# Kernel tuning notes

Hardware: AMD Instinct MI355X
Metric: run time of the kernel (lower is better)

The kernel has to match this reference:

```python
import jax, jax.numpy as jnp
import numpy as np

K = 3          # kernel size
PAD = 1        # padding
KK = K * K
RECURRENT = 3  # opt.Recurrent_times - 1


def dcnv2(x, offset, mask, weight, bias):
    """Modulated deformable conv (DCNv2), stride 1, pad 1, dilation 1.

    x:      [B, C, H, W]
    offset: [B, 2*KK, H, W]  -- (dy, dx) interleaved per kernel tap
    mask:   [B, KK, H, W]    -- modulation scalars
    weight: [O, C, K, K], bias: [O]
    """
    B, C, H, W = x.shape
    off = offset.reshape(B, KK, 2, H, W)
    dy, dx = off[:, :, 0], off[:, :, 1]                       # [B,KK,H,W]

    ky, kx = jnp.meshgrid(jnp.arange(K), jnp.arange(K), indexing='ij')
    ky = (ky.reshape(KK) - PAD).astype(x.dtype)               # {-1,0,1}
    kx = (kx.reshape(KK) - PAD).astype(x.dtype)
    iy = jnp.arange(H, dtype=x.dtype)
    ix = jnp.arange(W, dtype=x.dtype)

    # fractional sampling coords, [B,KK,H,W]
    py = iy[None, None, :, None] + ky[None, :, None, None] + dy
    px = ix[None, None, None, :] + kx[None, :, None, None] + dx

    y0 = jnp.floor(py)
    x0 = jnp.floor(px)
    wy = (py - y0)[:, None]                                   # [B,1,KK,H,W]
    wx = (px - x0)[:, None]

    x_flat = x.reshape(B, C, H * W)

    def gather(yi, xi):
        valid = ((yi >= 0) & (yi <= H - 1) & (xi >= 0) & (xi <= W - 1))
        yc = jnp.clip(yi, 0, H - 1).astype(jnp.int32)
        xc = jnp.clip(xi, 0, W - 1).astype(jnp.int32)
        idx = (yc * W + xc).reshape(B, -1)                    # [B, KK*H*W]
        g = jax.vmap(lambda im, id_: im[:, id_])(x_flat, idx)  # [B,C,KK*H*W]
        return g.reshape(B, C, KK, H, W) * valid.astype(x.dtype)[:, None]

    v00 = gather(y0, x0)
    v01 = gather(y0, x0 + 1)
    v10 = gather(y0 + 1, x0)
    v11 = gather(y0 + 1, x0 + 1)

    val = (v00 * (1 - wy) * (1 - wx) + v01 * (1 - wy) * wx
           + v10 * wy * (1 - wx) + v11 * wy * wx)
    val = val * mask[:, None]                                  # modulation

    out = jnp.einsum('ock,bckhw->bohw', weight.reshape(weight.shape[0], C, KK), val)
    return out + bias[None, :, None, None]


def setup_inputs() -> dict:
    key = jax.random.key(0)
    k1, k2, k3 = jax.random.split(key, 3)
    B, H, W = 4, 512, 512
    sharp = jax.random.normal(k1, (B, 3, H, W), dtype=jnp.float32)
    motion = jax.random.normal(k2, (B, 3 * KK, H, W), dtype=jnp.float32)
    # one 3x3x3->3 conv per recurrence, stacked: [RECURRENT, O, C, K, K]
    dcn_weights = jax.random.normal(k3, (RECURRENT, 3, 3, K, K), dtype=jnp.float32) * 0.1
    dcn_biases = jnp.zeros((RECURRENT, 3), dtype=jnp.float32)
    return {"sharp": sharp, "motion": motion,
            "dcn_weights": dcn_weights, "dcn_biases": dcn_biases}


def reference(sharp, motion, dcn_weights, dcn_biases):
    # torch.split(motion, [2*KK, KK], dim=1)
    offset = motion[:, :2 * KK]
    mask = motion[:, 2 * KK:]
    feats = [sharp]
    cur = sharp
    for i in range(RECURRENT):
        cur = dcnv2(cur, offset, mask, dcn_weights[i], dcn_biases[i])
        feats.append(cur)
    return sum(feats) / (RECURRENT + 1)
```

## Files before the change

kernel.cpp:

```cpp
#include <hip/hip_runtime.h>
#include <hip/hip_fp16.h>


#define HH 512
#define WW 512
#define BATCH 4
#define HWSZ (HH * WW)
#define PAIRS_PER_IMG (HWSZ / 2)

union U4 { uint4 u; __half2 h[4]; };
union U2 { uint2 u; __half2 h[2]; };

typedef const __attribute__((address_space(1))) void* gas_t;
typedef __attribute__((address_space(3))) void* las_t;

__global__ __launch_bounds__(256) void to_half_kernel(
    const float* __restrict__ sharp, uint4* __restrict__ dst)
{
    const int i = blockIdx.x * 256 + threadIdx.x;
    const int b = i >> 17;
    const int p = (i & (PAIRS_PER_IMG - 1)) * 2;
    const float* s = sharp + (size_t)b * 3 * HWSZ + p;
    const float2 c0 = *(const float2*)(s);
    const float2 c1 = *(const float2*)(s + HWSZ);
    const float2 c2 = *(const float2*)(s + 2 * HWSZ);
    U4 o;
    o.h[0] = __float22half2_rn(make_float2(c0.x, c1.x));
    o.h[1] = __float22half2_rn(make_float2(c2.x, 0.f));
    o.h[2] = __float22half2_rn(make_float2(c0.y, c1.y));
    o.h[3] = __float22half2_rn(make_float2(c2.y, 0.f));
    dst[i] = o.u;
}

__device__ __forceinline__ void bilinear3(const char* __restrict__ sb,
                                          float py, float px, float m,
                                          float& o0, float& o1, float& o2)
{
    const float y0f = floorf(py), x0f = floorf(px);
    const float wy = py - y0f, wx = px - x0f;
    const bool vy0 = (y0f >= 0.f) && (y0f <= 511.f);
    const bool vy1 = (y0f >= -1.f) && (y0f <= 510.f);
    const bool vx0 = (x0f >= 0.f) && (x0f <= 511.f);
    const bool vx1 = (x0f >= -1.f) && (x0f <= 510.f);
    const int iy0 = (int)fminf(fmaxf(y0f, 0.f), 511.f);
    const int iy1 = (int)fminf(fmaxf(y0f + 1.f, 0.f), 511.f);
    const int ix0 = (int)fminf(fmaxf(x0f, 0.f), 511.f);
    const int ix1 = (int)fminf(fmaxf(x0f + 1.f, 0.f), 511.f);
    const int lc  = (int)fminf(fmaxf(x0f, 0.f), 510.f);
    const int s0 = ix0 - lc;
    const int s1 = ix1 - lc;

    const float w00 = (vy0 && vx0) ? (1.f - wy) * (1.f - wx) * m : 0.f;
    const float w01 = (vy0 && vx1) ? (1.f - wy) * wx * m : 0.f;
    const float w10 = (vy1 && vx0) ? wy * (1.f - wx) * m : 0.f;
    const float w11 = (vy1 && vx1) ? wy * wx * m : 0.f;

    const float wlo0 = s0 ? 0.f : (s1 ? w00 : w00 + w01);
    const float whi0 = s1 ? (s0 ? w00 + w01 : w01) : 0.f;
    const float wlo1 = s0 ? 0.f : (s1 ? w10 : w10 + w11);
    const float whi1 = s1 ? (s0 ? w10 + w11 : w11) : 0.f;

    U4 ra, rb;
    ra.u = *(const uint4*)(sb + (size_t)(iy0 * WW + lc) * 8);
    rb.u = *(const uint4*)(sb + (size_t)(iy1 * WW + lc) * 8);
    const float2 aL = __half22float2(ra.h[0]);
    const float2 aLz = __half22float2(ra.h[1]);
    const float2 aH = __half22float2(ra.h[2]);
    const float2 aHz = __half22float2(ra.h[3]);
    const float2 bL = __half22float2(rb.h[0]);
    const float2 bLz = __half22float2(rb.h[1]);
    const float2 bH = __half22float2(rb.h[2]);
    const float2 bHz = __half22float2(rb.h[3]);

    o0 = wlo0 * aL.x + whi0 * aH.x + wlo1 * bL.x + whi1 * bH.x;
    o1 = wlo0 * aL.y + whi0 * aH.y + wlo1 * bL.y + whi1 * bH.y;
    o2 = wlo0 * aLz.x + whi0 * aHz.x + wlo1 * bLz.x + whi1 * bHz.x;
}

template <bool FIRST, bool WRITE_DST>
__global__ __launch_bounds__(256) void dcn_kernel(
    const uint2* __restrict__ src,
    const float* __restrict__ motion,
    const float* __restrict__ wgt,
    const float* __restrict__ bias,
    uint2* __restrict__ dst,
    float* __restrict__ out)
{
    __shared__ float mlds[27][256];
    __shared__ float sw[84];

    const int t = threadIdx.x;
    const int blk = blockIdx.x;
    const int b = blk >> 10;
    const int pbase = (blk & 1023) * 256;
    const int p = pbase + t;
    const int y = p >> 9;
    const int x = p & 511;

    if (t < 84) sw[t] = (t < 81) ? wgt[t] : bias[t - 81];

    {
        const int w = t >> 6, lane = t & 63;
        const float* mbase = motion + (size_t)b * 27 * HWSZ + pbase;
#pragma unroll
        for (int r = 0; r < 7; ++r) {
            const int plane = r * 4 + w;
            if (plane < 27) {
                const float* gsrc = mbase + (size_t)plane * HWSZ + lane * 4;
                __builtin_amdgcn_global_load_lds((gas_t)gsrc,
                                                 (las_t)&mlds[plane][0],
                                                 16, 0, 0);
            }
        }
    }
    __syncthreads();

    const char* sb = (const char*)src + (size_t)b * HWSZ * 8;

    float acc0 = sw[81], acc1 = sw[82], acc2 = sw[83];

#pragma unroll
    for (int k = 0; k < 9; ++k) {
        const float dy = mlds[2 * k][t];
        const float dx = mlds[2 * k + 1][t];
        const float m  = mlds[18 + k][t];
        const float py = (float)(y + k / 3 - 1) + dy;
        const float px = (float)(x + k % 3 - 1) + dx;

        float v0, v1, v2;
        bilinear3(sb, py, px, m, v0, v1, v2);
        acc0 += sw[0 * 9 + k] * v0 + sw[1 * 9 + k] * v1 + sw[2 * 9 + k] * v2;
        acc1 += sw[3 * 9 + k] * v0 + sw[4 * 9 + k] * v1 + sw[5 * 9 + k] * v2;
        acc2 += sw[6 * 9 + k] * v0 + sw[7 * 9 + k] * v1 + sw[8 * 9 + k] * v2;
    }

    if (WRITE_DST) {
        U2 o;
        o.h[0] = __float22half2_rn(make_float2(acc0, acc1));
        o.h[1] = __float22half2_rn(make_float2(acc2, 0.f));
        dst[(size_t)b * HWSZ + p] = o.u;
    }

    const size_t ob = (size_t)b * 3 * HWSZ + p;
    if (FIRST) {
        U2 c;
        c.u = *(const uint2*)(sb + (size_t)p * 8);
        const float2 s01 = __half22float2(c.h[0]);
        const float2 s2 = __half22float2(c.h[1]);
        out[ob] = (s01.x + acc0) * 0.25f;
        out[ob + HWSZ] = (s01.y + acc1) * 0.25f;
        out[ob + 2 * HWSZ] = (s2.x + acc2) * 0.25f;
    } else {
        out[ob] += acc0 * 0.25f;
        out[ob + HWSZ] += acc1 * 0.25f;
        out[ob + 2 * HWSZ] += acc2 * 0.25f;
    }
}

extern "C" void kernel_launch(void* const* d_in, const int* in_sizes, int n_in,
                              void* d_out, int out_size, void* d_ws, size_t ws_size,
                              hipStream_t stream) {
    const float* sharp  = (const float*)d_in[0];
    const float* motion = (const float*)d_in[1];
    const float* wts    = (const float*)d_in[2];
    const float* bias   = (const float*)d_in[3];
    float* out = (float*)d_out;

    uint2* bufA = (uint2*)d_ws;
    uint2* bufB = bufA + (size_t)BATCH * HWSZ;

    const dim3 block(256);
    const dim3 gridT(BATCH * PAIRS_PER_IMG / 256);
    const dim3 gridD(BATCH * HWSZ / 256);

    to_half_kernel<<<gridT, block, 0, stream>>>(sharp, (uint4*)bufA);
    dcn_kernel<true, true><<<gridD, block, 0, stream>>>(
        bufA, motion, wts, bias, bufB, out);
    dcn_kernel<false, true><<<gridD, block, 0, stream>>>(
        bufB, motion, wts + 81, bias + 3, bufA, out);
    dcn_kernel<false, false><<<gridD, block, 0, stream>>>(
        bufA, motion, wts + 162, bias + 6, nullptr, out);
}
```

Baseline: 119.5 us.

## Stage source halo tile in LDS and defer output accumulation to last pass

Each block now loads a 10x266 halo tile of the half-precision source image into shared memory and takes its bilinear samples from it, falling back to global loads when an offset points outside the tile. The output read-modify-write in every pass is replaced by writing three intermediate fp16 buffers, and the last pass sums them all into the output once. This cuts scattered global gather traffic and the repeated fp32 output reads and writes. In exchange it adds tile-loading work, more shared memory per block, a divergent fallback path, and extra fp16 buffer reads in the final pass.

```diff
diff --git a/kernel.cpp b/kernel.cpp
--- a/kernel.cpp
+++ b/kernel.cpp
@@ -6,7 +6,12 @@
 #define WW 512
 #define BATCH 4
 #define HWSZ (HH * WW)
-#define PAIRS_PER_IMG (HWSZ / 2)
+
+#define TROWS 10
+#define TCOLS 266
+#define TPITCH 272
+#define HALO_Y 4
+#define HALO_X 5
 
 union U4 { uint4 u; __half2 h[4]; };
 union U2 { uint2 u; __half2 h[2]; };
@@ -19,7 +24,7 @@
 {
     const int i = blockIdx.x * 256 + threadIdx.x;
     const int b = i >> 17;
-    const int p = (i & (PAIRS_PER_IMG - 1)) * 2;
+    const int p = (i & (HWSZ / 2 - 1)) * 2;
     const float* s = sharp + (size_t)b * 3 * HWSZ + p;
     const float2 c0 = *(const float2*)(s);
     const float2 c1 = *(const float2*)(s + HWSZ);
@@ -32,70 +37,29 @@
     dst[i] = o.u;
 }
 
-__device__ __forceinline__ void bilinear3(const char* __restrict__ sb,
-                                          float py, float px, float m,
-                                          float& o0, float& o1, float& o2)
-{
-    const float y0f = floorf(py), x0f = floorf(px);
-    const float wy = py - y0f, wx = px - x0f;
-    const bool vy0 = (y0f >= 0.f) && (y0f <= 511.f);
-    const bool vy1 = (y0f >= -1.f) && (y0f <= 510.f);
-    const bool vx0 = (x0f >= 0.f) && (x0f <= 511.f);
-    const bool vx1 = (x0f >= -1.f) && (x0f <= 510.f);
-    const int iy0 = (int)fminf(fmaxf(y0f, 0.f), 511.f);
-    const int iy1 = (int)fminf(fmaxf(y0f + 1.f, 0.f), 511.f);
-    const int ix0 = (int)fminf(fmaxf(x0f, 0.f), 511.f);
-    const int ix1 = (int)fminf(fmaxf(x0f + 1.f, 0.f), 511.f);
-    const int lc  = (int)fminf(fmaxf(x0f, 0.f), 510.f);
-    const int s0 = ix0 - lc;
-    const int s1 = ix1 - lc;
-
-    const float w00 = (vy0 && vx0) ? (1.f - wy) * (1.f - wx) * m : 0.f;
-    const float w01 = (vy0 && vx1) ? (1.f - wy) * wx * m : 0.f;
-    const float w10 = (vy1 && vx0) ? wy * (1.f - wx) * m : 0.f;
-    const float w11 = (vy1 && vx1) ? wy * wx * m : 0.f;
-
-    const float wlo0 = s0 ? 0.f : (s1 ? w00 : w00 + w01);
-    const float whi0 = s1 ? (s0 ? w00 + w01 : w01) : 0.f;
-    const float wlo1 = s0 ? 0.f : (s1 ? w10 : w10 + w11);
-    const float whi1 = s1 ? (s0 ? w10 + w11 : w11) : 0.f;
-
-    U4 ra, rb;
-    ra.u = *(const uint4*)(sb + (size_t)(iy0 * WW + lc) * 8);
-    rb.u = *(const uint4*)(sb + (size_t)(iy1 * WW + lc) * 8);
-    const float2 aL = __half22float2(ra.h[0]);
-    const float2 aLz = __half22float2(ra.h[1]);
-    const float2 aH = __half22float2(ra.h[2]);
-    const float2 aHz = __half22float2(ra.h[3]);
-    const float2 bL = __half22float2(rb.h[0]);
-    const float2 bLz = __half22float2(rb.h[1]);
-    const float2 bH = __half22float2(rb.h[2]);
-    const float2 bHz = __half22float2(rb.h[3]);
-
-    o0 = wlo0 * aL.x + whi0 * aH.x + wlo1 * bL.x + whi1 * bH.x;
-    o1 = wlo0 * aL.y + whi0 * aH.y + wlo1 * bL.y + whi1 * bH.y;
-    o2 = wlo0 * aLz.x + whi0 * aHz.x + wlo1 * bLz.x + whi1 * bHz.x;
-}
-
-template <bool FIRST, bool WRITE_DST>
-__global__ __launch_bounds__(256) void dcn_kernel(
+template <bool LAST>
+__global__ __launch_bounds__(256, 3) void dcn_kernel(
     const uint2* __restrict__ src,
     const float* __restrict__ motion,
     const float* __restrict__ wgt,
     const float* __restrict__ bias,
     uint2* __restrict__ dst,
+    const uint2* __restrict__ cS,
+    const uint2* __restrict__ c1,
     float* __restrict__ out)
 {
     __shared__ float mlds[27][256];
+    __shared__ U2 tile[TROWS * TPITCH];
     __shared__ float sw[84];
 
     const int t = threadIdx.x;
     const int blk = blockIdx.x;
     const int b = blk >> 10;
     const int pbase = (blk & 1023) * 256;
+    const int y = pbase >> 9;
+    const int xbase = pbase & 511;
+    const int x = xbase + t;
     const int p = pbase + t;
-    const int y = p >> 9;
-    const int x = p & 511;
 
     if (t < 84) sw[t] = (t < 81) ? wgt[t] : bias[t - 81];
 
@@ -113,9 +77,32 @@
             }
         }
     }
+
+    const uint2* simg = src + (size_t)b * HWSZ;
+
+#pragma unroll
+    for (int tr = 0; tr < TROWS; ++tr) {
+        const int gy = y - HALO_Y + tr;
+        if (gy >= 0 && gy < HH) {
+            int gx = xbase - HALO_X + t;
+            if (gx >= 0 && gx < WW)
+                tile[tr * TPITCH + t] = *(const U2*)&simg[gy * WW + gx];
+            if (t < TCOLS - 256) {
+                gx = xbase - HALO_X + 256 + t;
+                if (gx < WW)
+                    tile[tr * TPITCH + 256 + t] = *(const U2*)&simg[gy * WW + gx];
+            }
+        }
+    }
+
+    U2 csv, c1v, c2v;
+    if (LAST) {
+        csv = *(const U2*)&cS[(size_t)b * HWSZ + p];
+        c1v = *(const U2*)&c1[(size_t)b * HWSZ + p];
+        c2v = *(const U2*)&simg[p];
+    }
+
     __syncthreads();
-
-    const char* sb = (const char*)src + (size_t)b * HWSZ * 8;
 
     float acc0 = sw[81], acc1 = sw[82], acc2 = sw[83];
 
@@ -127,33 +114,81 @@
         const float py = (float)(y + k / 3 - 1) + dy;
         const float px = (float)(x + k % 3 - 1) + dx;
 
-        float v0, v1, v2;
-        bilinear3(sb, py, px, m, v0, v1, v2);
+        const float y0f = floorf(py), x0f = floorf(px);
+        const float wy = py - y0f, wx = px - x0f;
+        const bool vy0 = (y0f >= 0.f) && (y0f <= 511.f);
+        const bool vy1 = (y0f >= -1.f) && (y0f <= 510.f);
+        const bool vx0 = (x0f >= 0.f) && (x0f <= 511.f);
+        const bool vx1 = (x0f >= -1.f) && (x0f <= 510.f);
+        const int iy0 = (int)fminf(fmaxf(y0f, 0.f), 511.f);
+        const int iy1 = (int)fminf(fmaxf(y0f + 1.f, 0.f), 511.f);
+        const int ix0 = (int)fminf(fmaxf(x0f, 0.f), 511.f);
+        const int ix1 = (int)fminf(fmaxf(x0f + 1.f, 0.f), 511.f);
+        const int lc  = (int)fminf(fmaxf(x0f, 0.f), 510.f);
+        const int s0 = ix0 - lc, s1 = ix1 - lc;
+
+        const float w00 = (vy0 && vx0) ? (1.f - wy) * (1.f - wx) * m : 0.f;
+        const float w01 = (vy0 && vx1) ? (1.f - wy) * wx * m : 0.f;
+        const float w10 = (vy1 && vx0) ? wy * (1.f - wx) * m : 0.f;
+        const float w11 = (vy1 && vx1) ? wy * wx * m : 0.f;
+        const float wlo0 = s0 ? 0.f : (s1 ? w00 : w00 + w01);
+        const float whi0 = s1 ? (s0 ? w00 + w01 : w01) : 0.f;
+        const float wlo1 = s0 ? 0.f : (s1 ? w10 : w10 + w11);
+        const float whi1 = s1 ? (s0 ? w10 + w11 : w11) : 0.f;
+
+        U2 aL, aH, bL, bH;
+        const bool fast = (iy0 >= y - HALO_Y) && (iy1 <= y - HALO_Y + TROWS - 1) &&
+                          (lc >= xbase - HALO_X) && (lc <= xbase - HALO_X + TCOLS - 2);
+        if (fast) {
+            const int ta = (iy0 - (y - HALO_Y)) * TPITCH + (lc - (xbase - HALO_X));
+            const int tb = (iy1 - (y - HALO_Y)) * TPITCH + (lc - (xbase - HALO_X));
+            aL = tile[ta]; aH = tile[ta + 1];
+            bL = tile[tb]; bH = tile[tb + 1];
+        } else {
+            const char* sb = (const char*)simg;
+            U4 ra, rb;
+            ra.u = *(const uint4*)(sb + (size_t)(iy0 * WW + lc) * 8);
+            rb.u = *(const uint4*)(sb + (size_t)(iy1 * WW + lc) * 8);
+            aL.h[0] = ra.h[0]; aL.h[1] = ra.h[1];
+            aH.h[0] = ra.h[2]; aH.h[1] = ra.h[3];
+            bL.h[0] = rb.h[0]; bL.h[1] = rb.h[1];
+            bH.h[0] = rb.h[2]; bH.h[1] = rb.h[3];
+        }
+
+        const float2 aL01 = __half22float2(aL.h[0]);
+        const float2 aL2  = __half22float2(aL.h[1]);
+        const float2 aH01 = __half22float2(aH.h[0]);
+        const float2 aH2  = __half22float2(aH.h[1]);
+        const float2 bL01 = __half22float2(bL.h[0]);
+        const float2 bL2  = __half22float2(bL.h[1]);
+        const float2 bH01 = __half22float2(bH.h[0]);
+        const float2 bH2  = __half22float2(bH.h[1]);
+
+        const float v0 = wlo0 * aL01.x + whi0 * aH01.x + wlo1 * bL01.x + whi1 * bH01.x;
+        const float v1 = wlo0 * aL01.y + whi0 * aH01.y + wlo1 * bL01.y + whi1 * bH01.y;
+        const float v2 = wlo0 * aL2.x  + whi0 * aH2.x  + wlo1 * bL2.x  + whi1 * bH2.x;
+
         acc0 += sw[0 * 9 + k] * v0 + sw[1 * 9 + k] * v1 + sw[2 * 9 + k] * v2;
         acc1 += sw[3 * 9 + k] * v0 + sw[4 * 9 + k] * v1 + sw[5 * 9 + k] * v2;
         acc2 += sw[6 * 9 + k] * v0 + sw[7 * 9 + k] * v1 + sw[8 * 9 + k] * v2;
     }
 
-    if (WRITE_DST) {
+    if (!LAST) {
         U2 o;
         o.h[0] = __float22half2_rn(make_float2(acc0, acc1));
         o.h[1] = __float22half2_rn(make_float2(acc2, 0.f));
         dst[(size_t)b * HWSZ + p] = o.u;
-    }
-
-    const size_t ob = (size_t)b * 3 * HWSZ + p;
-    if (FIRST) {
-        U2 c;
-        c.u = *(const uint2*)(sb + (size_t)p * 8);
-        const float2 s01 = __half22float2(c.h[0]);
-        const float2 s2 = __half22float2(c.h[1]);
-        out[ob] = (s01.x + acc0) * 0.25f;
-        out[ob + HWSZ] = (s01.y + acc1) * 0.25f;
-        out[ob + 2 * HWSZ] = (s2.x + acc2) * 0.25f;
     } else {
-        out[ob] += acc0 * 0.25f;
-        out[ob + HWSZ] += acc1 * 0.25f;
-        out[ob + 2 * HWSZ] += acc2 * 0.25f;
+        const float2 s01 = __half22float2(csv.h[0]);
+        const float2 s2  = __half22float2(csv.h[1]);
+        const float2 a01 = __half22float2(c1v.h[0]);
+        const float2 a2  = __half22float2(c1v.h[1]);
+        const float2 b01 = __half22float2(c2v.h[0]);
+        const float2 b2  = __half22float2(c2v.h[1]);
+        const size_t ob = (size_t)b * 3 * HWSZ + p;
+        out[ob]             = (s01.x + a01.x + b01.x + acc0) * 0.25f;
+        out[ob + HWSZ]      = (s01.y + a01.y + b01.y + acc1) * 0.25f;
+        out[ob + 2 * HWSZ]  = (s2.x  + a2.x  + b2.x  + acc2) * 0.25f;
     }
 }
 
@@ -166,18 +201,20 @@
     const float* bias   = (const float*)d_in[3];
     float* out = (float*)d_out;
 
-    uint2* bufA = (uint2*)d_ws;
-    uint2* bufB = bufA + (size_t)BATCH * HWSZ;
+    const size_t img = (size_t)BATCH * HWSZ;
+    uint2* bufS = (uint2*)d_ws;
+    uint2* buf1 = bufS + img;
+    uint2* buf2 = buf1 + img;
 
     const dim3 block(256);
-    const dim3 gridT(BATCH * PAIRS_PER_IMG / 256);
-    const dim3 gridD(BATCH * HWSZ / 256);
-
-    to_half_kernel<<<gridT, block, 0, stream>>>(sharp, (uint4*)bufA);
-    dcn_kernel<true, true><<<gridD, block, 0, stream>>>(
-        bufA, motion, wts, bias, bufB, out);
-    dcn_kernel<false, true><<<gridD, block, 0, stream>>>(
-        bufB, motion, wts + 81, bias + 3, bufA, out);
-    dcn_kernel<false, false><<<gridD, block, 0, stream>>>(
-        bufA, motion, wts + 162, bias + 6, nullptr, out);
+    const dim3 gridT(img / 512);
+    const dim3 gridD(img / 256);
+
+    to_half_kernel<<<gridT, block, 0, stream>>>(sharp, (uint4*)bufS);
+    dcn_kernel<false><<<gridD, block, 0, stream>>>(
+        bufS, motion, wts, bias, buf1, nullptr, nullptr, nullptr);
+    dcn_kernel<false><<<gridD, block, 0, stream>>>(
+        buf1, motion, wts + 81, bias + 3, buf2, nullptr, nullptr, nullptr);
+    dcn_kernel<true><<<gridD, block, 0, stream>>>(
+        buf2, motion, wts + 162, bias + 6, nullptr, bufS, buf1, out);
 }
```

Measured after the change: 399.3 us. +234.2%, slower.

## Repack motion to fp16 once and defer output accumulation to last pass

Applied to the files above, without the earlier changes.

The first DCN pass converts the fp32 offset/mask planes it already stages in LDS into an fp16 copy in workspace. Later passes load that half-size copy instead of re-reading the fp32 motion tensor. The per-pass read-modify-write of the fp32 output is removed: intermediate results stay in fp16 buffers, and the final pass sums sharp, pass-1, pass-2 and its own result and writes the output once. This cuts global traffic but quantizes offsets and masks to fp16, which loses sampling-coordinate precision at large pixel coordinates, and the first pass now writes an extra fp16 motion copy.

```diff
diff --git a/kernel.cpp b/kernel.cpp
--- a/kernel.cpp
+++ b/kernel.cpp
@@ -6,7 +6,7 @@
 #define WW 512
 #define BATCH 4
 #define HWSZ (HH * WW)
-#define PAIRS_PER_IMG (HWSZ / 2)
+#define MP 28
 
 union U4 { uint4 u; __half2 h[4]; };
 union U2 { uint2 u; __half2 h[2]; };
@@ -19,7 +19,7 @@
 {
     const int i = blockIdx.x * 256 + threadIdx.x;
     const int b = i >> 17;
-    const int p = (i & (PAIRS_PER_IMG - 1)) * 2;
+    const int p = (i & (HWSZ / 2 - 1)) * 2;
     const float* s = sharp + (size_t)b * 3 * HWSZ + p;
     const float2 c0 = *(const float2*)(s);
     const float2 c1 = *(const float2*)(s + HWSZ);
@@ -77,53 +77,103 @@
     o2 = wlo0 * aLz.x + whi0 * aHz.x + wlo1 * bLz.x + whi1 * bHz.x;
 }
 
-template <bool FIRST, bool WRITE_DST>
+template <bool FP16MOT, bool REPACK, bool LAST>
 __global__ __launch_bounds__(256) void dcn_kernel(
     const uint2* __restrict__ src,
     const float* __restrict__ motion,
+    __half* __restrict__ mot16,
     const float* __restrict__ wgt,
     const float* __restrict__ bias,
     uint2* __restrict__ dst,
+    const uint2* __restrict__ cS,
+    const uint2* __restrict__ c1,
     float* __restrict__ out)
 {
-    __shared__ float mlds[27][256];
+    __shared__ __align__(16) char msmem[FP16MOT ? MP * 256 * 2 : 27 * 256 * 4];
     __shared__ float sw[84];
 
     const int t = threadIdx.x;
     const int blk = blockIdx.x;
     const int b = blk >> 10;
     const int pbase = (blk & 1023) * 256;
+    const int y = pbase >> 9;
+    const int x = (pbase & 511) + t;
     const int p = pbase + t;
-    const int y = p >> 9;
-    const int x = p & 511;
+    const int w = t >> 6, lane = t & 63;
 
     if (t < 84) sw[t] = (t < 81) ? wgt[t] : bias[t - 81];
 
-    {
-        const int w = t >> 6, lane = t & 63;
+    if (!FP16MOT) {
         const float* mbase = motion + (size_t)b * 27 * HWSZ + pbase;
 #pragma unroll
         for (int r = 0; r < 7; ++r) {
-            const int plane = r * 4 + w;
-            if (plane < 27) {
-                const float* gsrc = mbase + (size_t)plane * HWSZ + lane * 4;
+            const int pl = r * 4 + w;
+            if (pl < 27) {
+                const float* gsrc = mbase + (size_t)pl * HWSZ + lane * 4;
                 __builtin_amdgcn_global_load_lds((gas_t)gsrc,
-                                                 (las_t)&mlds[plane][0],
+                                                 (las_t)(msmem + pl * 1024),
                                                  16, 0, 0);
             }
         }
-    }
+    } else {
+        const __half* mbase = mot16 + (size_t)b * MP * HWSZ + pbase;
+#pragma unroll
+        for (int r = 0; r < 4; ++r) {
+            const int q = r * 4 + w;
+            if (q < 14) {
+                const int pl = 2 * q + (lane >> 5);
+                const __half* gsrc = mbase + (size_t)pl * HWSZ + (lane & 31) * 8;
+                __builtin_amdgcn_global_load_lds((gas_t)gsrc,
+                                                 (las_t)(msmem + q * 1024),
+                                                 16, 0, 0);
+            }
+        }
+    }
+
+    const uint2* simg = src + (size_t)b * HWSZ;
+
+    U2 csv, c1v, c2v;
+    if (LAST) {
+        csv = *(const U2*)&cS[(size_t)b * HWSZ + p];
+        c1v = *(const U2*)&c1[(size_t)b * HWSZ + p];
+        c2v = *(const U2*)&simg[p];
+    }
+
     __syncthreads();
 
-    const char* sb = (const char*)src + (size_t)b * HWSZ * 8;
-
+    if (REPACK) {
+        __half* obase = mot16 + (size_t)b * MP * HWSZ + pbase;
+        const float* mf = (const float*)msmem;
+#pragma unroll
+        for (int r = 0; r < 7; ++r) {
+            const int pl = r * 4 + w;
+            if (pl < 27) {
+                const float4 v = *(const float4*)&mf[pl * 256 + lane * 4];
+                U2 o;
+                o.h[0] = __float22half2_rn(make_float2(v.x, v.y));
+                o.h[1] = __float22half2_rn(make_float2(v.z, v.w));
+                *(uint2*)(obase + (size_t)pl * HWSZ + lane * 4) = o.u;
+            }
+        }
+    }
+
+    const char* sb = (const char*)simg;
     float acc0 = sw[81], acc1 = sw[82], acc2 = sw[83];
 
 #pragma unroll
     for (int k = 0; k < 9; ++k) {
-        const float dy = mlds[2 * k][t];
-        const float dx = mlds[2 * k + 1][t];
-        const float m  = mlds[18 + k][t];
+        float dy, dx, m;
+        if (!FP16MOT) {
+            const float* mf = (const float*)msmem;
+            dy = mf[(2 * k) * 256 + t];
+            dx = mf[(2 * k + 1) * 256 + t];
+            m  = mf[(18 + k) * 256 + t];
+        } else {
+            const __half* mh = (const __half*)msmem;
+            dy = __half2float(mh[(2 * k) * 256 + t]);
+            dx = __half2float(mh[(2 * k + 1) * 256 + t]);
+            m  = __half2float(mh[(18 + k) * 256 + t]);
+        }
         const float py = (float)(y + k / 3 - 1) + dy;
         const float px = (float)(x + k % 3 - 1) + dx;
 
@@ -134,26 +184,22 @@
         acc2 += sw[6 * 9 + k] * v0 + sw[7 * 9 + k] * v1 + sw[8 * 9 + k] * v2;
     }
 
-    if (WRITE_DST) {
+    if (!LAST) {
         U2 o;
         o.h[0] = __float22half2_rn(make_float2(acc0, acc1));
         o.h[1] = __float22half2_rn(make_float2(acc2, 0.f));
         dst[(size_t)b * HWSZ + p] = o.u;
-    }
-
-    const size_t ob = (size_t)b * 3 * HWSZ + p;
-    if (FIRST) {
-        U2 c;
-        c.u = *(const uint2*)(sb + (size_t)p * 8);
-        const float2 s01 = __half22float2(c.h[0]);
-        const float2 s2 = __half22float2(c.h[1]);
-        out[ob] = (s01.x + acc0) * 0.25f;
-        out[ob + HWSZ] = (s01.y + acc1) * 0.25f;
-        out[ob + 2 * HWSZ] = (s2.x + acc2) * 0.25f;
     } else {
-        out[ob] += acc0 * 0.25f;
-        out[ob + HWSZ] += acc1 * 0.25f;
-        out[ob + 2 * HWSZ] += acc2 * 0.25f;
+        const float2 s01 = __half22float2(csv.h[0]);
+        const float2 s2  = __half22float2(csv.h[1]);
+        const float2 a01 = __half22float2(c1v.h[0]);
+        const float2 a2  = __half22float2(c1v.h[1]);
+        const float2 b01 = __half22float2(c2v.h[0]);
+        const float2 b2  = __half22float2(c2v.h[1]);
+        const size_t ob = (size_t)b * 3 * HWSZ + p;
+        out[ob]            = (s01.x + a01.x + b01.x + acc0) * 0.25f;
+        out[ob + HWSZ]     = (s01.y + a01.y + b01.y + acc1) * 0.25f;
+        out[ob + 2 * HWSZ] = (s2.x  + a2.x  + b2.x  + acc2) * 0.25f;
     }
 }
 
@@ -166,18 +212,21 @@
     const float* bias   = (const float*)d_in[3];
     float* out = (float*)d_out;
 
-    uint2* bufA = (uint2*)d_ws;
-    uint2* bufB = bufA + (size_t)BATCH * HWSZ;
+    const size_t img = (size_t)BATCH * HWSZ;
+    uint2* bufS = (uint2*)d_ws;
+    uint2* buf1 = bufS + img;
+    uint2* buf2 = buf1 + img;
+    __half* mot16 = (__half*)(buf2 + img);
 
     const dim3 block(256);
-    const dim3 gridT(BATCH * PAIRS_PER_IMG / 256);
-    const dim3 gridD(BATCH * HWSZ / 256);
-
-    to_half_kernel<<<gridT, block, 0, stream>>>(sharp, (uint4*)bufA);
-    dcn_kernel<true, true><<<gridD, block, 0, stream>>>(
-        bufA, motion, wts, bias, bufB, out);
-    dcn_kernel<false, true><<<gridD, block, 0, stream>>>(
-        bufB, motion, wts + 81, bias + 3, bufA, out);
-    dcn_kernel<false, false><<<gridD, block, 0, stream>>>(
-        bufA, motion, wts + 162, bias + 6, nullptr, out);
-}
+    const dim3 gridT(img / 512);
+    const dim3 gridD(img / 256);
+
+    to_half_kernel<<<gridT, block, 0, stream>>>(sharp, (uint4*)bufS);
+    dcn_kernel<false, true, false><<<gridD, block, 0, stream>>>(
+        bufS, motion, mot16, wts, bias, buf1, nullptr, nullptr, nullptr);
+    dcn_kernel<true, false, false><<<gridD, block, 0, stream>>>(
+        buf1, nullptr, mot16, wts + 81, bias + 3, buf2, nullptr, nullptr, nullptr);
+    dcn_kernel<true, false, true><<<gridD, block, 0, stream>>>(
+        buf2, nullptr, mot16, wts + 162, bias + 6, nullptr, bufS, buf1, out);
+}
```

Result: no change. 117.3 us (-1.9%).

## Defer output accumulation to last pass and double-buffer motion loads per block

Applied to the files above, without the earlier changes.

Each block now processes two 256-pixel strips. The second strip's motion planes are prefetched into a separate LDS buffer while the first strip is computed. The fp32 output read-modify-write in every pass is replaced by keeping all intermediate features in a third half-precision buffer, so only the final pass reads the three saved features and writes the averaged output once. This removes two full fp32 output read/write passes but adds a third workspace buffer, doubles LDS use (which can lower occupancy), and halves the number of blocks.

```diff
diff --git a/kernel.cpp b/kernel.cpp
--- a/kernel.cpp
+++ b/kernel.cpp
@@ -6,7 +6,6 @@
 #define WW 512
 #define BATCH 4
 #define HWSZ (HH * WW)
-#define PAIRS_PER_IMG (HWSZ / 2)
 
 union U4 { uint4 u; __half2 h[4]; };
 union U2 { uint2 u; __half2 h[2]; };
@@ -19,7 +18,7 @@
 {
     const int i = blockIdx.x * 256 + threadIdx.x;
     const int b = i >> 17;
-    const int p = (i & (PAIRS_PER_IMG - 1)) * 2;
+    const int p = (i & (HWSZ / 2 - 1)) * 2;
     const float* s = sharp + (size_t)b * 3 * HWSZ + p;
     const float2 c0 = *(const float2*)(s);
     const float2 c1 = *(const float2*)(s + HWSZ);
@@ -77,83 +76,134 @@
     o2 = wlo0 * aLz.x + whi0 * aHz.x + wlo1 * bLz.x + whi1 * bHz.x;
 }
 
-template <bool FIRST, bool WRITE_DST>
+__device__ __forceinline__ void dcn_strip(
+    const float* __restrict__ mf, const float* __restrict__ sw,
+    const char* __restrict__ sb, int y, int x,
+    float& acc0, float& acc1, float& acc2)
+{
+    acc0 = sw[81]; acc1 = sw[82]; acc2 = sw[83];
+#pragma unroll
+    for (int k = 0; k < 9; ++k) {
+        const float dy = mf[(2 * k) * 256];
+        const float dx = mf[(2 * k + 1) * 256];
+        const float m  = mf[(18 + k) * 256];
+        const float py = (float)(y + k / 3 - 1) + dy;
+        const float px = (float)(x + k % 3 - 1) + dx;
+
+        float v0, v1, v2;
+        bilinear3(sb, py, px, m, v0, v1, v2);
+        acc0 += sw[0 * 9 + k] * v0 + sw[1 * 9 + k] * v1 + sw[2 * 9 + k] * v2;
+        acc1 += sw[3 * 9 + k] * v0 + sw[4 * 9 + k] * v1 + sw[5 * 9 + k] * v2;
+        acc2 += sw[6 * 9 + k] * v0 + sw[7 * 9 + k] * v1 + sw[8 * 9 + k] * v2;
+    }
+}
+
+template <bool LAST>
 __global__ __launch_bounds__(256) void dcn_kernel(
     const uint2* __restrict__ src,
     const float* __restrict__ motion,
     const float* __restrict__ wgt,
     const float* __restrict__ bias,
     uint2* __restrict__ dst,
+    const uint2* __restrict__ cS,
+    const uint2* __restrict__ c1,
     float* __restrict__ out)
 {
-    __shared__ float mlds[27][256];
+    __shared__ __align__(16) float mlds0[27 * 256];
+    __shared__ __align__(16) float mlds1[27 * 256];
     __shared__ float sw[84];
 
     const int t = threadIdx.x;
     const int blk = blockIdx.x;
-    const int b = blk >> 10;
-    const int pbase = (blk & 1023) * 256;
-    const int p = pbase + t;
-    const int y = p >> 9;
-    const int x = p & 511;
+    const int s0i = blk * 2;
+    const int b = s0i >> 10;
+    const int pb0 = (s0i & 1023) * 256;
+    const int pb1 = pb0 + 256;
+    const int y = pb0 >> 9;
+    const int w = t >> 6, lane = t & 63;
 
     if (t < 84) sw[t] = (t < 81) ? wgt[t] : bias[t - 81];
 
-    {
-        const int w = t >> 6, lane = t & 63;
-        const float* mbase = motion + (size_t)b * 27 * HWSZ + pbase;
+    const float* mbase = motion + (size_t)b * 27 * HWSZ;
+
 #pragma unroll
-        for (int r = 0; r < 7; ++r) {
-            const int plane = r * 4 + w;
-            if (plane < 27) {
-                const float* gsrc = mbase + (size_t)plane * HWSZ + lane * 4;
-                __builtin_amdgcn_global_load_lds((gas_t)gsrc,
-                                                 (las_t)&mlds[plane][0],
-                                                 16, 0, 0);
-            }
+    for (int r = 0; r < 7; ++r) {
+        const int pl = r * 4 + w;
+        if (pl < 27) {
+            __builtin_amdgcn_global_load_lds(
+                (gas_t)(mbase + (size_t)pl * HWSZ + pb0 + lane * 4),
+                (las_t)(mlds0 + pl * 256), 16, 0, 0);
         }
     }
+
     __syncthreads();
 
-    const char* sb = (const char*)src + (size_t)b * HWSZ * 8;
-
-    float acc0 = sw[81], acc1 = sw[82], acc2 = sw[83];
-
 #pragma unroll
-    for (int k = 0; k < 9; ++k) {
-        const float dy = mlds[2 * k][t];
-        const float dx = mlds[2 * k + 1][t];
-        const float m  = mlds[18 + k][t];
-        const float py = (float)(y + k / 3 - 1) + dy;
-        const float px = (float)(x + k % 3 - 1) + dx;
-
-        float v0, v1, v2;
-        bilinear3(sb, py, px, m, v0, v1, v2);
-        acc0 += sw[0 * 9 + k] * v0 + sw[1 * 9 + k] * v1 + sw[2 * 9 + k] * v2;
-        acc1 += sw[3 * 9 + k] * v0 + sw[4 * 9 + k] * v1 + sw[5 * 9 + k] * v2;
-        acc2 += sw[6 * 9 + k] * v0 + sw[7 * 9 + k] * v1 + sw[8 * 9 + k] * v2;
-    }
-
-    if (WRITE_DST) {
+    for (int r = 0; r < 7; ++r) {
+        const int pl = r * 4 + w;
+        if (pl < 27) {
+            __builtin_amdgcn_global_load_lds(
+                (gas_t)(mbase + (size_t)pl * HWSZ + pb1 + lane * 4),
+                (las_t)(mlds1 + pl * 256), 16, 0, 0);
+        }
+    }
+
+    const uint2* simg = src + ((size_t)b << 18);
+    const char* sb = (const char*)simg;
+    const int p0 = pb0 + t, p1 = pb1 + t;
+
+    U2 cs0, c10, c20, cs1, c11, c21;
+    if (LAST) {
+        cs0 = *(const U2*)&cS[((size_t)b << 18) + p0];
+        c10 = *(const U2*)&c1[((size_t)b << 18) + p0];
+        c20 = *(const U2*)&simg[p0];
+        cs1 = *(const U2*)&cS[((size_t)b << 18) + p1];
+        c11 = *(const U2*)&c1[((size_t)b << 18) + p1];
+        c21 = *(const U2*)&simg[p1];
+    }
+
+    float a0, a1, a2;
+    dcn_strip(mlds0 + t, sw, sb, y, t, a0, a1, a2);
+
+    if (!LAST) {
         U2 o;
-        o.h[0] = __float22half2_rn(make_float2(acc0, acc1));
-        o.h[1] = __float22half2_rn(make_float2(acc2, 0.f));
-        dst[(size_t)b * HWSZ + p] = o.u;
-    }
-
-    const size_t ob = (size_t)b * 3 * HWSZ + p;
-    if (FIRST) {
-        U2 c;
-        c.u = *(const uint2*)(sb + (size_t)p * 8);
-        const float2 s01 = __half22float2(c.h[0]);
-        const float2 s2 = __half22float2(c.h[1]);
-        out[ob] = (s01.x + acc0) * 0.25f;
-        out[ob + HWSZ] = (s01.y + acc1) * 0.25f;
-        out[ob + 2 * HWSZ] = (s2.x + acc2) * 0.25f;
+        o.h[0] = __float22half2_rn(make_float2(a0, a1));
+        o.h[1] = __float22half2_rn(make_float2(a2, 0.f));
+        dst[((size_t)b << 18) + p0] = o.u;
     } else {
-        out[ob] += acc0 * 0.25f;
-        out[ob + HWSZ] += acc1 * 0.25f;
-        out[ob + 2 * HWSZ] += acc2 * 0.25f;
+        const float2 s01 = __half22float2(cs0.h[0]);
+        const float2 s2  = __half22float2(cs0.h[1]);
+        const float2 f101 = __half22float2(c10.h[0]);
+        const float2 f12  = __half22float2(c10.h[1]);
+        const float2 f201 = __half22float2(c20.h[0]);
+        const float2 f22  = __half22float2(c20.h[1]);
+        const size_t ob = (size_t)b * 3 * HWSZ + p0;
+        out[ob]            = (s01.x + f101.x + f201.x + a0) * 0.25f;
+        out[ob + HWSZ]     = (s01.y + f101.y + f201.y + a1) * 0.25f;
+        out[ob + 2 * HWSZ] = (s2.x  + f12.x  + f22.x  + a2) * 0.25f;
+    }
+
+    __syncthreads();
+
+    float b0, b1, b2;
+    dcn_strip(mlds1 + t, sw, sb, y, 256 + t, b0, b1, b2);
+
+    if (!LAST) {
+        U2 o;
+        o.h[0] = __float22half2_rn(make_float2(b0, b1));
+        o.h[1] = __float22half2_rn(make_float2(b2, 0.f));
+        dst[((size_t)b << 18) + p1] = o.u;
+    } else {
+        const float2 s01 = __half22float2(cs1.h[0]);
+        const float2 s2  = __half22float2(cs1.h[1]);
+        const float2 f101 = __half22float2(c11.h[0]);
+        const float2 f12  = __half22float2(c11.h[1]);
+        const float2 f201 = __half22float2(c21.h[0]);
+        const float2 f22  = __half22float2(c21.h[1]);
+        const size_t ob = (size_t)b * 3 * HWSZ + p1;
+        out[ob]            = (s01.x + f101.x + f201.x + b0) * 0.25f;
+        out[ob + HWSZ]     = (s01.y + f101.y + f201.y + b1) * 0.25f;
+        out[ob + 2 * HWSZ] = (s2.x  + f12.x  + f22.x  + b2) * 0.25f;
     }
 }
 
@@ -166,18 +216,20 @@
     const float* bias   = (const float*)d_in[3];
     float* out = (float*)d_out;
 
-    uint2* bufA = (uint2*)d_ws;
-    uint2* bufB = bufA + (size_t)BATCH * HWSZ;
+    const size_t img = (size_t)BATCH * HWSZ;
+    uint2* bufS = (uint2*)d_ws;
+    uint2* buf1 = bufS + img;
+    uint2* buf2 = buf1 + img;
 
     const dim3 block(256);
-    const dim3 gridT(BATCH * PAIRS_PER_IMG / 256);
-    const dim3 gridD(BATCH * HWSZ / 256);
-
-    to_half_kernel<<<gridT, block, 0, stream>>>(sharp, (uint4*)bufA);
-    dcn_kernel<true, true><<<gridD, block, 0, stream>>>(
-        bufA, motion, wts, bias, bufB, out);
-    dcn_kernel<false, true><<<gridD, block, 0, stream>>>(
-        bufB, motion, wts + 81, bias + 3, bufA, out);
-    dcn_kernel<false, false><<<gridD, block, 0, stream>>>(
-        bufA, motion, wts + 162, bias + 6, nullptr, out);
-}
+    const dim3 gridT(img / 512);
+    const dim3 gridD(img / 512);
+
+    to_half_kernel<<<gridT, block, 0, stream>>>(sharp, (uint4*)bufS);
+    dcn_kernel<false><<<gridD, block, 0, stream>>>(
+        bufS, motion, wts, bias, buf1, nullptr, nullptr, nullptr);
+    dcn_kernel<false><<<gridD, block, 0, stream>>>(
+        buf1, motion, wts + 81, bias + 3, buf2, nullptr, nullptr, nullptr);
+    dcn_kernel<true><<<gridD, block, 0, stream>>>(
+        buf2, motion, wts + 162, bias + 6, nullptr, bufS, buf1, out);
+}
```

Result: slower. 147.0 us (+23.0%).
